# Kernel optimization log

Measured on AMD Instinct MI355X. Metric: run time of the kernel, lower is better.

The kernel has to match this reference:

```python
import jax, jax.numpy as jnp
import numpy as np
import math

B, S, D, H, M, R = 4, 1024, 1024, 16, 4, 64
DH = D // H
EPS = 1e-8

def setup_inputs() -> dict:
    key = jax.random.key(0)
    ks = jax.random.split(key, 8)
    sc = 0.02
    return {
        'x': jax.random.normal(ks[0], (B, S, D), jnp.float32),
        'Wk': jax.random.normal(ks[1], (D, D), jnp.float32) * sc,
        'bk': jnp.zeros((D,), jnp.float32),
        'Wq': jax.random.normal(ks[2], (D, D), jnp.float32) * sc,
        'bq': jnp.zeros((D,), jnp.float32),
        'Wv': jax.random.normal(ks[3], (D, D), jnp.float32) * sc,
        'bv': jnp.zeros((D,), jnp.float32),
        'mask1': jax.random.normal(ks[4], (M, R, S), jnp.float32) * sc,
        'mask2': jax.random.normal(ks[5], (M, R, S), jnp.float32) * sc,
        'roll_back': jax.random.randint(ks[6], (M, S, S), 0, S, jnp.int64),
    }

def reference(x, Wk, bk, Wq, bq, Wv, bv, mask1, mask2, roll_back):
    def proj(W, b):
        # torch Linear: x @ W^T + b ; reshape to [B, H, S, DH]
        y = jnp.dot(x, W.T) + b
        return y.reshape(B, S, H, DH).transpose(0, 2, 1, 3)
    k = proj(Wk, bk)
    q = proj(Wq, bq)
    v = proj(Wv, bv)
    # learnable low-rank mask: [M, S, S]
    learnable_mask = jnp.einsum('mrs,mrt->mst', mask1, mask2)
    # gather along last dim with roll_back indices
    gathered = jnp.take_along_axis(learnable_mask, roll_back, axis=-1)  # [M, S, S]
    att = jnp.einsum('bhsd,bhtd->bhst', q, k) / math.sqrt(DH)  # [B, H, S, S]
    att = att.reshape(B, H // M, M, S, S) * gathered[None, None]
    att = att.reshape(B, H, S, S)
    # Frobenius norm over last two dims per (B, H)
    fro = jnp.sqrt(jnp.sum(att * att, axis=(-2, -1), keepdims=True))
    att = att / (fro + EPS)
    out = jnp.einsum('bhst,bhtd->bhsd', att, v)
    return out.transpose(0, 2, 1, 3).reshape(B, S, D)
```

## Files before the change

kernel.cpp:

```cpp
#include <hip/hip_runtime.h>
#include <hip/hip_bf16.h>
#include <stdint.h>

typedef __attribute__((ext_vector_type(8))) __bf16 bf16x8;
typedef __attribute__((ext_vector_type(4))) float  f32x4;
typedef __attribute__((ext_vector_type(16))) float f32x16;

__device__ __forceinline__ ushort f2bf(float f) {
    union { float f; uint32_t u; } v; v.f = f;
    uint32_t u = v.u;
    uint32_t r = 0x7FFFu + ((u >> 16) & 1u);
    return (ushort)((u + r) >> 16);
}
__device__ __forceinline__ float bf2f(ushort u) {
    union { uint32_t u; float f; } v; v.u = ((uint32_t)u) << 16;
    return v.f;
}

typedef __attribute__((address_space(3))) uint32_t lds_u32_t;
typedef const __attribute__((address_space(1))) uint32_t glb_u32_t;
__device__ __forceinline__ void async_copy16(const void* g, void* l) {
    __builtin_amdgcn_global_load_lds((glb_u32_t*)g, (lds_u32_t*)l, 16, 0, 0);
}

__global__ __launch_bounds__(256) void convert_all(
    const float* __restrict__ x, const float* __restrict__ wk,
    const float* __restrict__ wq, const float* __restrict__ wv,
    ushort* __restrict__ xb, ushort* __restrict__ wball)
{
    int i = blockIdx.x * 256 + threadIdx.x;
    const float* src; ushort* dst; int j;
    if (i < 1048576) { src = x; dst = xb; j = i; }
    else {
        int t = i - 1048576;
        int z = t >> 18;
        j = t & 262143;
        src = (z == 0) ? wk : (z == 1) ? wq : wv;
        dst = wball + z * 1048576;
    }
    float4 f = ((const float4*)src)[j];
    ushort4 o;
    o.x = f2bf(f.x); o.y = f2bf(f.y); o.z = f2bf(f.z); o.w = f2bf(f.w);
    ((ushort4*)dst)[j] = o;
}

__global__ __launch_bounds__(256) void proj_gemm(
    const ushort* __restrict__ xb, const ushort* __restrict__ wball,
    const float* __restrict__ bk, const float* __restrict__ bq, const float* __restrict__ bv,
    ushort* __restrict__ kd, ushort* __restrict__ qd, ushort* __restrict__ vd)
{
    __shared__ ushort As[3 * 128 * 32];
    __shared__ ushort Bs[3 * 128 * 32];
    const int z = blockIdx.z;
    const int row0 = blockIdx.x * 128;
    const int col0 = blockIdx.y * 128;
    const ushort* wb = wball + z * 1048576;
    const int tid = threadIdx.x;
    const int lane = tid & 63, wave = tid >> 6;
    const int quad = lane >> 4, m15 = lane & 15;
    const int wr = wave >> 1, wc = wave & 1;

    f32x4 acc[4][4];
    for (int i = 0; i < 4; i++)
        for (int j = 0; j < 4; j++) acc[i][j] = (f32x4){0.f, 0.f, 0.f, 0.f};

#define STAGE(BI, KK) do {                                                        \
        _Pragma("unroll")                                                         \
        for (int i_ = 0; i_ < 2; i_++) {                                          \
            int c_ = tid + i_ * 256;                                  \
            int r_ = c_ >> 2, cjp_ = c_ & 3;                                      \
            int cj_ = cjp_ ^ ((r_ >> 1) & 3);                                     \
            async_copy16(&xb[(row0 + r_) * 1024 + (KK) + cj_ * 8],                \
                         &As[(BI) * 4096 + c_ * 8]);                              \
            async_copy16(&wb[(col0 + r_) * 1024 + (KK) + cj_ * 8],                \
                         &Bs[(BI) * 4096 + c_ * 8]);                              \
        }                                                                         \
    } while (0)

#define COMPUTE(BI) do {                                                          \
        const ushort* a_ = &As[(BI) * 4096];                                      \
        const ushort* b_ = &Bs[(BI) * 4096];                                      \
        bf16x8 af[4], bfv[4];                                                     \
        _Pragma("unroll")                                                         \
        for (int fr = 0; fr < 4; fr++) {                                          \
            int row = wr * 64 + fr * 16 + m15;                                    \
            af[fr] = *(const bf16x8*)&a_[row * 32 + ((quad ^ ((row >> 1) & 3)) * 8)]; \
        }                                                                         \
        _Pragma("unroll")                                                         \
        for (int fc = 0; fc < 4; fc++) {                                          \
            int row = wc * 64 + fc * 16 + m15;                                    \
            bfv[fc] = *(const bf16x8*)&b_[row * 32 + ((quad ^ ((row >> 1) & 3)) * 8)]; \
        }                                                                         \
        _Pragma("unroll")                                                         \
        for (int fr = 0; fr < 4; fr++)                                            \
            _Pragma("unroll")                                                     \
            for (int fc = 0; fc < 4; fc++)                                        \
                acc[fr][fc] = __builtin_amdgcn_mfma_f32_16x16x32_bf16(            \
                    af[fr], bfv[fc], acc[fr][fc], 0, 0, 0);                       \
    } while (0)

    STAGE(0, 0);
    STAGE(1, 32);

    int cur = 0;
    #pragma unroll 3
    for (int t = 0; t < 30; ++t) {
        int sb = cur + 2; if (sb >= 3) sb -= 3;
        STAGE(sb, (t + 2) * 32);
        asm volatile("s_waitcnt vmcnt(8)" ::: "memory");
        __builtin_amdgcn_s_barrier();
        COMPUTE(cur);
        __builtin_amdgcn_s_barrier();
        cur = (cur == 2) ? 0 : cur + 1;
    }
    asm volatile("s_waitcnt vmcnt(4)" ::: "memory");
    __builtin_amdgcn_s_barrier();
    COMPUTE(cur);
    cur = (cur == 2) ? 0 : cur + 1;
    asm volatile("s_waitcnt vmcnt(0)" ::: "memory");
    __builtin_amdgcn_s_barrier();
    COMPUTE(cur);

#undef STAGE
#undef COMPUTE

    const float* bias = (z == 0) ? bk : (z == 1) ? bq : bv;
    ushort* dstA = (z == 0) ? kd : qd;
    for (int fr = 0; fr < 4; fr++) {
        int ibase = row0 + wr * 64 + fr * 16 + quad * 4;
        int b_ = ibase >> 10, s = ibase & 1023;
        for (int fc = 0; fc < 4; fc++) {
            int j = col0 + wc * 64 + fc * 16 + m15;
            int h = j >> 6, dh = j & 63;
            float bb = bias[j];
            if (z < 2) {
                for (int r = 0; r < 4; r++)
                    dstA[((b_ * 16 + h) * 1024 + (s + r)) * 64 + dh] = f2bf(acc[fr][fc][r] + bb);
            } else {
                ushort4 o;
                o.x = f2bf(acc[fr][fc][0] + bb);
                o.y = f2bf(acc[fr][fc][1] + bb);
                o.z = f2bf(acc[fr][fc][2] + bb);
                o.w = f2bf(acc[fr][fc][3] + bb);
                *(ushort4*)&vd[((b_ * 16 + h) * 64 + dh) * 1024 + s] = o;
            }
        }
    }
}

__global__ __launch_bounds__(256) void mask_fused(
    const float* __restrict__ m1, const float* __restrict__ m2,
    const int* __restrict__ rb, ushort* __restrict__ gth)
{
    __shared__ float As8[64 * 8];
    __shared__ float lmS[8 * 1024];
    const int s0 = blockIdx.x * 8;
    const int m = blockIdx.y;
    const int tid = threadIdx.x;

    if (tid < 128) {
        int r = tid >> 1, half = tid & 1;
        *(float4*)&As8[r * 8 + half * 4] =
            *(const float4*)&m1[(m * 64 + r) * 1024 + s0 + half * 4];
    }
    __syncthreads();

    f32x4 acc8[8];
    #pragma unroll
    for (int s = 0; s < 8; s++) acc8[s] = (f32x4){0.f, 0.f, 0.f, 0.f};
    const float* m2b = m2 + m * 65536 + tid * 4;
    #pragma unroll 4
    for (int r = 0; r < 64; r++) {
        float4 b4 = *(const float4*)&m2b[r * 1024];
        f32x4 b = (f32x4){b4.x, b4.y, b4.z, b4.w};
        #pragma unroll
        for (int s = 0; s < 8; s++) {
            float a = As8[r * 8 + s];
            acc8[s] += a * b;
        }
    }
    #pragma unroll
    for (int s = 0; s < 8; s++)
        *(f32x4*)&lmS[s * 1024 + tid * 4] = acc8[s];
    __syncthreads();

    const int base = (m * 1024 + s0) * 1024;
    #pragma unroll
    for (int i = 0; i < 8; i++) {
        int c = tid + i * 256;
        int row = c >> 8, j = (c & 255) * 4;
        int4 idx = *(const int4*)&rb[base + row * 1024 + j];
        ushort4 o;
        o.x = f2bf(lmS[row * 1024 + (idx.x & 1023)] * 0.125f);
        o.y = f2bf(lmS[row * 1024 + (idx.y & 1023)] * 0.125f);
        o.z = f2bf(lmS[row * 1024 + (idx.z & 1023)] * 0.125f);
        o.w = f2bf(lmS[row * 1024 + (idx.w & 1023)] * 0.125f);
        *(ushort4*)&gth[base + row * 1024 + j] = o;
    }
}

__global__ __launch_bounds__(256, 4) void attention(
    const ushort* __restrict__ qd, const ushort* __restrict__ kd, const ushort* __restrict__ vd,
    const ushort* __restrict__ gth, float* __restrict__ O, float* __restrict__ ss)
{
    __shared__ ushort Ks[64 * 72];
    __shared__ ushort Vs[64 * 72];
    __shared__ ushort Ps[64 * 72];
    __shared__ ushort Ms[64 * 72];
    __shared__ float red[4];
    const int s0 = blockIdx.x * 64;
    const int bh = blockIdx.y;
    const int mm = bh & 3;
    const int tid = threadIdx.x, lane = tid & 63, wave = tid >> 6;
    const int l31 = lane & 31, hl = lane >> 5;
    const int wr2 = wave >> 1, wc2 = wave & 1;

    const int r0_ = tid >> 3,          o0_ = (tid & 7) * 8;
    const int r1_ = (tid + 256) >> 3,  o1_ = ((tid + 256) & 7) * 8;

    const ushort* gbase = gth + mm * 1048576 + s0 * 1024;
    const ushort* kdb = kd + bh * 65536;
    const ushort* vdb = vd + bh * 65536;

    *(uint4*)&Ms[r0_ * 72 + o0_] = *(const uint4*)&qd[(bh * 1024 + s0 + r0_) * 64 + o0_];
    *(uint4*)&Ms[r1_ * 72 + o1_] = *(const uint4*)&qd[(bh * 1024 + s0 + r1_) * 64 + o1_];
    uint4 kr0, kr1, vr0, vr1, mr0, mr1;
    kr0 = *(const uint4*)&kdb[r0_ * 64 + o0_];
    kr1 = *(const uint4*)&kdb[r1_ * 64 + o1_];
    vr0 = *(const uint4*)&vdb[r0_ * 1024 + o0_];
    vr1 = *(const uint4*)&vdb[r1_ * 1024 + o1_];
    mr0 = *(const uint4*)&gbase[r0_ * 1024 + o0_];
    mr1 = *(const uint4*)&gbase[r1_ * 1024 + o1_];
    __syncthreads();
    bf16x8 qf[4];
    #pragma unroll
    for (int kk = 0; kk < 4; kk++)
        qf[kk] = *(const bf16x8*)&Ms[(wr2 * 32 + l31) * 72 + kk * 16 + hl * 8];
    __syncthreads();

    *(uint4*)&Ks[r0_ * 72 + o0_] = kr0;
    *(uint4*)&Ks[r1_ * 72 + o1_] = kr1;
    *(uint4*)&Vs[r0_ * 72 + o0_] = vr0;
    *(uint4*)&Vs[r1_ * 72 + o1_] = vr1;
    *(uint4*)&Ms[r0_ * 72 + o0_] = mr0;
    *(uint4*)&Ms[r1_ * 72 + o1_] = mr1;
    kr0 = *(const uint4*)&kdb[(64 + r0_) * 64 + o0_];
    kr1 = *(const uint4*)&kdb[(64 + r1_) * 64 + o1_];
    vr0 = *(const uint4*)&vdb[r0_ * 1024 + 64 + o0_];
    vr1 = *(const uint4*)&vdb[r1_ * 1024 + 64 + o1_];
    mr0 = *(const uint4*)&gbase[r0_ * 1024 + 64 + o0_];
    mr1 = *(const uint4*)&gbase[r1_ * 1024 + 64 + o1_];
    __syncthreads();

    f32x16 oacc;
    #pragma unroll
    for (int i = 0; i < 16; i++) oacc[i] = 0.f;
    float ssacc = 0.f;

    for (int t = 0; t < 16; ++t) {
        f32x16 p;
        #pragma unroll
        for (int i = 0; i < 16; i++) p[i] = 0.f;
        #pragma unroll
        for (int kk = 0; kk < 4; kk++) {
            bf16x8 b = *(const bf16x8*)&Ks[(wc2 * 32 + l31) * 72 + kk * 16 + hl * 8];
            p = __builtin_amdgcn_mfma_f32_32x32x16_bf16(qf[kk], b, p, 0, 0, 0);
        }
        {
            const int col = wc2 * 32 + l31;
            #pragma unroll
            for (int reg = 0; reg < 16; reg++) {
                int row = wr2 * 32 + (reg & 3) + 8 * (reg >> 2) + 4 * hl;
                float pv = p[reg] * bf2f(Ms[row * 72 + col]);
                ssacc += pv * pv;
                Ps[row * 72 + col] = f2bf(pv);
            }
        }
        __syncthreads();
        #pragma unroll
        for (int kk = 0; kk < 4; kk++) {
            bf16x8 a = *(const bf16x8*)&Ps[(wr2 * 32 + l31) * 72 + kk * 16 + hl * 8];
            bf16x8 b = *(const bf16x8*)&Vs[(wc2 * 32 + l31) * 72 + kk * 16 + hl * 8];
            oacc = __builtin_amdgcn_mfma_f32_32x32x16_bf16(a, b, oacc, 0, 0, 0);
        }
        __syncthreads();
        if (t < 15) {
            *(uint4*)&Ks[r0_ * 72 + o0_] = kr0;
            *(uint4*)&Ks[r1_ * 72 + o1_] = kr1;
            *(uint4*)&Vs[r0_ * 72 + o0_] = vr0;
            *(uint4*)&Vs[r1_ * 72 + o1_] = vr1;
            *(uint4*)&Ms[r0_ * 72 + o0_] = mr0;
            *(uint4*)&Ms[r1_ * 72 + o1_] = mr1;
            if (t < 14) {
                const int tn = (t + 2) * 64;
                kr0 = *(const uint4*)&kdb[(tn + r0_) * 64 + o0_];
                kr1 = *(const uint4*)&kdb[(tn + r1_) * 64 + o1_];
                vr0 = *(const uint4*)&vdb[r0_ * 1024 + tn + o0_];
                vr1 = *(const uint4*)&vdb[r1_ * 1024 + tn + o1_];
                mr0 = *(const uint4*)&gbase[r0_ * 1024 + tn + o0_];
                mr1 = *(const uint4*)&gbase[r1_ * 1024 + tn + o1_];
            }
            __syncthreads();
        }
    }
    #pragma unroll
    for (int reg = 0; reg < 16; reg++) {
        int s = s0 + wr2 * 32 + (reg & 3) + 8 * (reg >> 2) + 4 * hl;
        int dh = wc2 * 32 + l31;
        O[(bh * 1024 + s) * 64 + dh] = oacc[reg];
    }
    for (int off = 32; off; off >>= 1) ssacc += __shfl_down(ssacc, off, 64);
    if (lane == 0) red[wave] = ssacc;
    __syncthreads();
    if (tid == 0) atomicAdd(&ss[bh], red[0] + red[1] + red[2] + red[3]);
}

__global__ __launch_bounds__(256) void normalize_out(const float* __restrict__ O,
                                                     const float* __restrict__ ss,
                                                     float* __restrict__ out)
{
    int gid = blockIdx.x * 256 + threadIdx.x;
    int e = gid * 4;
    int bh = e >> 16;
    float inv = 1.f / (sqrtf(ss[bh]) + 1e-8f);
    float4 v4 = *(const float4*)&O[e];
    int b_ = bh >> 4, h = bh & 15;
    int s = (e >> 6) & 1023, dh = e & 63;
    float4 o4 = {v4.x * inv, v4.y * inv, v4.z * inv, v4.w * inv};
    *(float4*)&out[((b_ * 1024 + s) * 16 + h) * 64 + dh] = o4;
}

extern "C" void kernel_launch(void* const* d_in, const int* in_sizes, int n_in,
                              void* d_out, int out_size, void* d_ws, size_t ws_size,
                              hipStream_t stream) {
    const float* x  = (const float*)d_in[0];
    const float* Wk = (const float*)d_in[1];
    const float* bk = (const float*)d_in[2];
    const float* Wq = (const float*)d_in[3];
    const float* bq = (const float*)d_in[4];
    const float* Wv = (const float*)d_in[5];
    const float* bv = (const float*)d_in[6];
    const float* m1 = (const float*)d_in[7];
    const float* m2 = (const float*)d_in[8];
    const int*   rb = (const int*)d_in[9];
    float* out = (float*)d_out;

    char* ws = (char*)d_ws;
    ushort* xb    = (ushort*)(ws);
    ushort* wball = (ushort*)(ws + 8388608);
    ushort* kd    = (ushort*)(ws + 14680064);
    ushort* qd    = (ushort*)(ws + 23068672);
    ushort* vd    = (ushort*)(ws + 31457280);
    float*  O     = (float*)(ws + 39845888);
    ushort* gth   = (ushort*)(ws + 56623104);
    float*  ssb   = (float*)(ws + 65011712);

    convert_all<<<7168, 256, 0, stream>>>(x, Wk, Wq, Wv, xb, wball);
    proj_gemm<<<dim3(32, 8, 3), 256, 0, stream>>>(xb, wball, bk, bq, bv, kd, qd, vd);
    mask_fused<<<dim3(128, 4), 256, 0, stream>>>(m1, m2, rb, gth);
    hipMemsetAsync(ssb, 0, 64 * sizeof(float), stream);
    attention<<<dim3(16, 64), 256, 0, stream>>>(qd, kd, vd, gth, O, ssb);
    normalize_out<<<4096, 256, 0, stream>>>(O, ssb, out);
}
```

Measured before the change: 195.3 us.

## Load gathered mask directly into registers and transpose QK MFMA operands

```diff
diff --git a/kernel.cpp b/kernel.cpp
--- a/kernel.cpp
+++ b/kernel.cpp
@@ -206,7 +206,6 @@
     __shared__ ushort Ks[64 * 72];
     __shared__ ushort Vs[64 * 72];
     __shared__ ushort Ps[64 * 72];
-    __shared__ ushort Ms[64 * 72];
     __shared__ float red[4];
     const int s0 = blockIdx.x * 64;
     const int bh = blockIdx.y;
@@ -218,44 +217,44 @@
     const int r0_ = tid >> 3,          o0_ = (tid & 7) * 8;
     const int r1_ = (tid + 256) >> 3,  o1_ = ((tid + 256) & 7) * 8;
 
-    const ushort* gbase = gth + mm * 1048576 + s0 * 1024;
     const ushort* kdb = kd + bh * 65536;
     const ushort* vdb = vd + bh * 65536;
 
-    *(uint4*)&Ms[r0_ * 72 + o0_] = *(const uint4*)&qd[(bh * 1024 + s0 + r0_) * 64 + o0_];
-    *(uint4*)&Ms[r1_ * 72 + o1_] = *(const uint4*)&qd[(bh * 1024 + s0 + r1_) * 64 + o1_];
-    uint4 kr0, kr1, vr0, vr1, mr0, mr1;
-    kr0 = *(const uint4*)&kdb[r0_ * 64 + o0_];
-    kr1 = *(const uint4*)&kdb[r1_ * 64 + o1_];
-    vr0 = *(const uint4*)&vdb[r0_ * 1024 + o0_];
-    vr1 = *(const uint4*)&vdb[r1_ * 1024 + o1_];
-    mr0 = *(const uint4*)&gbase[r0_ * 1024 + o0_];
-    mr1 = *(const uint4*)&gbase[r1_ * 1024 + o1_];
+    const int srow = wr2 * 32 + l31;
+    const int tb   = wc2 * 32 + 4 * hl;
+    const ushort* grow = gth + mm * 1048576 + (s0 + srow) * 1024 + tb;
+
+    *(uint4*)&Ks[r0_ * 72 + o0_] = *(const uint4*)&qd[(bh * 1024 + s0 + r0_) * 64 + o0_];
+    *(uint4*)&Ks[r1_ * 72 + o1_] = *(const uint4*)&qd[(bh * 1024 + s0 + r1_) * 64 + o1_];
+    uint4 kr0 = *(const uint4*)&kdb[r0_ * 64 + o0_];
+    uint4 kr1 = *(const uint4*)&kdb[r1_ * 64 + o1_];
+    uint4 vr0 = *(const uint4*)&vdb[r0_ * 1024 + o0_];
+    uint4 vr1 = *(const uint4*)&vdb[r1_ * 1024 + o1_];
+    ushort4 mk0 = *(const ushort4*)&grow[0];
+    ushort4 mk1 = *(const ushort4*)&grow[8];
+    ushort4 mk2 = *(const ushort4*)&grow[16];
+    ushort4 mk3 = *(const ushort4*)&grow[24];
     __syncthreads();
     bf16x8 qf[4];
     #pragma unroll
     for (int kk = 0; kk < 4; kk++)
-        qf[kk] = *(const bf16x8*)&Ms[(wr2 * 32 + l31) * 72 + kk * 16 + hl * 8];
+        qf[kk] = *(const bf16x8*)&Ks[srow * 72 + kk * 16 + hl * 8];
     __syncthreads();
 
     *(uint4*)&Ks[r0_ * 72 + o0_] = kr0;
     *(uint4*)&Ks[r1_ * 72 + o1_] = kr1;
     *(uint4*)&Vs[r0_ * 72 + o0_] = vr0;
     *(uint4*)&Vs[r1_ * 72 + o1_] = vr1;
-    *(uint4*)&Ms[r0_ * 72 + o0_] = mr0;
-    *(uint4*)&Ms[r1_ * 72 + o1_] = mr1;
     kr0 = *(const uint4*)&kdb[(64 + r0_) * 64 + o0_];
     kr1 = *(const uint4*)&kdb[(64 + r1_) * 64 + o1_];
     vr0 = *(const uint4*)&vdb[r0_ * 1024 + 64 + o0_];
     vr1 = *(const uint4*)&vdb[r1_ * 1024 + 64 + o1_];
-    mr0 = *(const uint4*)&gbase[r0_ * 1024 + 64 + o0_];
-    mr1 = *(const uint4*)&gbase[r1_ * 1024 + 64 + o1_];
     __syncthreads();
 
     f32x16 oacc;
     #pragma unroll
     for (int i = 0; i < 16; i++) oacc[i] = 0.f;
-    float ssacc = 0.f;
+    float ss0 = 0.f, ss1 = 0.f, ss2 = 0.f, ss3 = 0.f;
 
     for (int t = 0; t < 16; ++t) {
         f32x16 p;
@@ -263,18 +262,29 @@
         for (int i = 0; i < 16; i++) p[i] = 0.f;
         #pragma unroll
         for (int kk = 0; kk < 4; kk++) {
-            bf16x8 b = *(const bf16x8*)&Ks[(wc2 * 32 + l31) * 72 + kk * 16 + hl * 8];
-            p = __builtin_amdgcn_mfma_f32_32x32x16_bf16(qf[kk], b, p, 0, 0, 0);
-        }
-        {
-            const int col = wc2 * 32 + l31;
-            #pragma unroll
-            for (int reg = 0; reg < 16; reg++) {
-                int row = wr2 * 32 + (reg & 3) + 8 * (reg >> 2) + 4 * hl;
-                float pv = p[reg] * bf2f(Ms[row * 72 + col]);
-                ssacc += pv * pv;
-                Ps[row * 72 + col] = f2bf(pv);
-            }
+            bf16x8 kf = *(const bf16x8*)&Ks[(wc2 * 32 + l31) * 72 + kk * 16 + hl * 8];
+            p = __builtin_amdgcn_mfma_f32_32x32x16_bf16(kf, qf[kk], p, 0, 0, 0);
+        }
+#define MBLK(G, MK) do {                                               \
+            float pv0 = p[4*(G)+0] * bf2f((MK).x);                     \
+            float pv1 = p[4*(G)+1] * bf2f((MK).y);                     \
+            float pv2 = p[4*(G)+2] * bf2f((MK).z);                     \
+            float pv3 = p[4*(G)+3] * bf2f((MK).w);                     \
+            ss0 += pv0 * pv0; ss1 += pv1 * pv1;                        \
+            ss2 += pv2 * pv2; ss3 += pv3 * pv3;                        \
+            ushort4 o_;                                                \
+            o_.x = f2bf(pv0); o_.y = f2bf(pv1);                        \
+            o_.z = f2bf(pv2); o_.w = f2bf(pv3);                        \
+            *(ushort4*)&Ps[srow * 72 + tb + 8 * (G)] = o_;             \
+        } while (0)
+        MBLK(0, mk0); MBLK(1, mk1); MBLK(2, mk2); MBLK(3, mk3);
+#undef MBLK
+        if (t < 15) {
+            const ushort* gn = grow + (t + 1) * 64;
+            mk0 = *(const ushort4*)&gn[0];
+            mk1 = *(const ushort4*)&gn[8];
+            mk2 = *(const ushort4*)&gn[16];
+            mk3 = *(const ushort4*)&gn[24];
         }
         __syncthreads();
         #pragma unroll
@@ -289,16 +299,12 @@
             *(uint4*)&Ks[r1_ * 72 + o1_] = kr1;
             *(uint4*)&Vs[r0_ * 72 + o0_] = vr0;
             *(uint4*)&Vs[r1_ * 72 + o1_] = vr1;
-            *(uint4*)&Ms[r0_ * 72 + o0_] = mr0;
-            *(uint4*)&Ms[r1_ * 72 + o1_] = mr1;
             if (t < 14) {
                 const int tn = (t + 2) * 64;
                 kr0 = *(const uint4*)&kdb[(tn + r0_) * 64 + o0_];
                 kr1 = *(const uint4*)&kdb[(tn + r1_) * 64 + o1_];
                 vr0 = *(const uint4*)&vdb[r0_ * 1024 + tn + o0_];
                 vr1 = *(const uint4*)&vdb[r1_ * 1024 + tn + o1_];
-                mr0 = *(const uint4*)&gbase[r0_ * 1024 + tn + o0_];
-                mr1 = *(const uint4*)&gbase[r1_ * 1024 + tn + o1_];
             }
             __syncthreads();
         }
@@ -309,6 +315,7 @@
         int dh = wc2 * 32 + l31;
         O[(bh * 1024 + s) * 64 + dh] = oacc[reg];
     }
+    float ssacc = (ss0 + ss1) + (ss2 + ss3);
     for (int off = 32; off; off >>= 1) ssacc += __shfl_down(ssacc, off, 64);
     if (lane == 0) red[wave] = ssacc;
     __syncthreads();
```

New measurement: 195.9 us. No clear change (+0.3%).
